# Kernel tuning notes

Hardware: AMD Instinct MI355X
Metric: run time of the kernel (lower is better)

Reference implementation:

```python
import jax, jax.numpy as jnp
import numpy as np

Y = 1      # init kwarg y
DIM = 2    # init kwarg dim


def setup_inputs() -> dict:
    key = jax.random.key(0)
    k1, k2, k3 = jax.random.split(key, 3)
    B, L = 16, 512
    H = 32
    x = jax.random.normal(k1, (B, L, L), dtype=jnp.float32)
    # xavier_uniform-like init for weights
    lim1 = np.sqrt(6.0 / (3 + H)).astype(np.float32)
    W1 = jax.random.uniform(k2, (H, 3), dtype=jnp.float32, minval=-lim1, maxval=lim1)
    b1 = jnp.zeros((H,), dtype=jnp.float32)
    lim2 = np.sqrt(6.0 / (H + 1)).astype(np.float32)
    W2 = jax.random.uniform(k3, (1, H), dtype=jnp.float32, minval=-lim2, maxval=lim2)
    b2 = jnp.zeros((1,), dtype=jnp.float32)
    return {"x": x, "W1": W1, "b1": b1, "W2": W2, "b2": b2}


def reference(x, W1, b1, W2, b2):
    # nearest-neighbor sum along both lattice dims
    x1 = (jnp.roll(x, 1, axis=1) + jnp.roll(x, -1, axis=1)
          + jnp.roll(x, 1, axis=2) + jnp.roll(x, -1, axis=2))
    # shifted-by-y neighbor sum along DIM
    sx = jnp.roll(x, Y, axis=DIM) + jnp.roll(x, -Y, axis=DIM)
    # per-site 3-feature vector: [x^2, x1*x, sx*x] -> (B, L, L, 3)
    inp = jnp.stack([x * x, x1 * x, sx * x], axis=-1)
    # tiny pointwise MLP 3 -> 32 -> 1
    h = jnp.tanh(jnp.einsum('blmf,hf->blmh', inp, W1) + b1)
    out = jnp.einsum('blmh,oh->blmo', h, W2)[..., 0] + b2[0]
    # sum over lattice sites -> per-config scalar (B,)
    return out.sum(axis=(1, 2))
```

## Files before the change

### kernel.cpp

```cpp
#include <hip/hip_runtime.h>

#define L 512
#define LMASK 511
#define HID 32

constexpr int THREADS        = 256;
constexpr int ROWS_PER_BLOCK = 4;
constexpr int BLOCKS_PER_B   = L / ROWS_PER_BLOCK;
constexpr int NTAB           = 680;
constexpr float UCLAMP_HI    = 672.99f;

__global__ __launch_bounds__(THREADS, 4)
void site_kernel(const float* __restrict__ x,
                 const float* __restrict__ W1,
                 const float* __restrict__ b1,
                 const float* __restrict__ W2,
                 float* __restrict__ partial) {
    __shared__ __align__(16) float  zw_s[128];
    __shared__ __align__(16) float  w2_s[HID];
    __shared__ __align__(8)  float2 tab_s[NTAB];

    const int t = threadIdx.x;

    if (t < HID) {
        const float K16 = 16.0f * 2.8853900817779268f;
        const int g = t >> 2, q = t & 3;
        zw_s[g * 16 +  0 + q] = K16 * W1[t * 3 + 0];
        zw_s[g * 16 +  4 + q] = K16 * W1[t * 3 + 1];
        zw_s[g * 16 +  8 + q] = K16 * W1[t * 3 + 2];
        zw_s[g * 16 + 12 + q] = fmaf(K16, b1[t], 336.0f);
        w2_s[t] = -2.0f * W2[t];
    }
    for (int i = t; i < NTAB; i += THREADS) {
        const float z0 = fmaf((float)i, 0.0625f, -21.0f);
        const float v0 = 1.0f / (1.0f + __builtin_amdgcn_exp2f(z0));
        const float v1 = 1.0f / (1.0f + __builtin_amdgcn_exp2f(z0 + 0.0625f));
        const float s  = v1 - v0;
        tab_s[i] = make_float2(s, fmaf(-s, (float)i, v0));
    }
    __syncthreads();

    const int blk = blockIdx.x;
    const int b   = blk >> 7;
    const int i0  = (blk & (BLOCKS_PER_B - 1)) * ROWS_PER_BLOCK;
    const float* __restrict__ xb = x + (size_t)b * (L * L);

    float F0[8], F1[8], F2[8];
#pragma unroll
    for (int g = 0; g < 2; ++g) {
        const int j  = t + g * THREADS;
        const int jm = (j + LMASK) & LMASK, jp = (j + 1) & LMASK;

        float cc[6];
#pragma unroll
        for (int r = 0; r < 6; ++r) {
            const int i = (i0 + r - 1 + L) & LMASK;
            cc[r] = xb[i * L + j];
        }
#pragma unroll
        for (int s = 0; s < 4; ++s) {
            const int i   = i0 + s;
            const float lf = xb[i * L + jm];
            const float rg = xb[i * L + jp];
            const float c  = cc[s + 1];
            const float lr = lf + rg;
            const float x1 = lr + cc[s] + cc[s + 2];
            const int k = g * 4 + s;
            F0[k] = c * c;  F1[k] = x1 * c;  F2[k] = lr * c;
        }
    }

    float acc[8] = {0.f, 0.f, 0.f, 0.f, 0.f, 0.f, 0.f, 0.f};

#pragma unroll 1
    for (int gq = 0; gq < 8; ++gq) {
        const float4 wa  = *(const float4*)&zw_s[gq * 16 + 0];
        const float4 wb  = *(const float4*)&zw_s[gq * 16 + 4];
        const float4 wc  = *(const float4*)&zw_s[gq * 16 + 8];
        const float4 w0  = *(const float4*)&zw_s[gq * 16 + 12];
        const float4 w2v = *(const float4*)&w2_s[gq * 4];
#pragma unroll
        for (int q = 0; q < 4; ++q) {
            const float waq = ((const float*)&wa)[q];
            const float wbq = ((const float*)&wb)[q];
            const float wcq = ((const float*)&wc)[q];
            const float w0q = ((const float*)&w0)[q];
            const float w2q = ((const float*)&w2v)[q];
#pragma unroll
            for (int s = 0; s < 8; ++s) {
                const float uu = fmaf(F0[s], waq, fmaf(F1[s], wbq, fmaf(F2[s], wcq, w0q)));
                const float uc = __builtin_amdgcn_fmed3f(uu, 0.0f, UCLAMP_HI);
                const int  idx = (int)uc;
                const float2 sa = tab_s[idx];
                acc[s] = fmaf(w2q, fmaf(sa.x, uc, sa.y), acc[s]);
            }
        }
    }

    float a = ((acc[0] + acc[1]) + (acc[2] + acc[3]))
            + ((acc[4] + acc[5]) + (acc[6] + acc[7]));
#pragma unroll
    for (int off = 32; off > 0; off >>= 1)
        a += __shfl_down(a, off, 64);

    __shared__ float wsum[THREADS / 64];
    const int wid = t >> 6, lane = t & 63;
    if (lane == 0) wsum[wid] = a;
    __syncthreads();
    if (t == 0)
        partial[blk] = (wsum[0] + wsum[1]) + (wsum[2] + wsum[3]);
}

__global__ __launch_bounds__(128)
void reduce_kernel(const float* __restrict__ partial,
                   const float* __restrict__ W2,
                   const float* __restrict__ b2,
                   float* __restrict__ out) {
    const int b = blockIdx.x, t = threadIdx.x;
    const float NS = (float)(L * L);

    float v = partial[b * BLOCKS_PER_B + t];
    if (t < HID) v += NS * W2[t];
    if (t == 0)  v += NS * b2[0];

#pragma unroll
    for (int off = 32; off > 0; off >>= 1)
        v += __shfl_down(v, off, 64);

    __shared__ float ws2[2];
    if ((t & 63) == 0) ws2[t >> 6] = v;
    __syncthreads();
    if (t == 0) out[b] = ws2[0] + ws2[1];
}

extern "C" void kernel_launch(void* const* d_in, const int* in_sizes, int n_in,
                              void* d_out, int out_size, void* d_ws, size_t ws_size,
                              hipStream_t stream) {
    const float* x  = (const float*)d_in[0];
    const float* W1 = (const float*)d_in[1];
    const float* b1 = (const float*)d_in[2];
    const float* W2 = (const float*)d_in[3];
    const float* b2 = (const float*)d_in[4];
    float* out      = (float*)d_out;
    float* partial  = (float*)d_ws;

    const int B = in_sizes[0] / (L * L);

    site_kernel<<<B * BLOCKS_PER_B, THREADS, 0, stream>>>(x, W1, b1, W2, partial);
    reduce_kernel<<<B, 128, 0, stream>>>(partial, W2, b2, out);
}
```

Measured before the change: 35.42 us.

## Replace interpolated tanh table with denser nearest-entry table via magic-number indexing

Swaps the 680-entry linear-interpolation sigmoid table for a 5376-entry nearest-neighbour table at 1/64 spacing. A magic-number bias (2^23) is added to the pre-activation so the table byte offset can be pulled straight from the float mantissa bits. This removes the float-to-int conversion, the float2 load and the interpolation FMA from the inner loop. In exchange, accuracy drops from linear interpolation to nearest-sample lookup, and shared memory use grows to about 21KB per block. The occupancy hint in launch_bounds is also removed.

```diff
diff --git a/kernel.cpp b/kernel.cpp
--- a/kernel.cpp
+++ b/kernel.cpp
@@ -7,36 +7,36 @@
 constexpr int THREADS        = 256;
 constexpr int ROWS_PER_BLOCK = 4;
 constexpr int BLOCKS_PER_B   = L / ROWS_PER_BLOCK;
-constexpr int NTAB           = 680;
-constexpr float UCLAMP_HI    = 672.99f;
+constexpr int NTAB           = 5376;
 
-__global__ __launch_bounds__(THREADS, 4)
+constexpr float MAGIC   = 8388608.0f;
+constexpr float CLAMPLO = 8388608.0f;
+constexpr float CLAMPHI = 8410108.0f;
+
+__global__ __launch_bounds__(THREADS)
 void site_kernel(const float* __restrict__ x,
                  const float* __restrict__ W1,
                  const float* __restrict__ b1,
                  const float* __restrict__ W2,
                  float* __restrict__ partial) {
-    __shared__ __align__(16) float  zw_s[128];
-    __shared__ __align__(16) float  w2_s[HID];
-    __shared__ __align__(8)  float2 tab_s[NTAB];
+    __shared__ __align__(16) float tab_s[NTAB];
+    __shared__ __align__(16) float zw_s[128];
+    __shared__ __align__(16) float w2_s[HID];
 
     const int t = threadIdx.x;
 
     if (t < HID) {
-        const float K16 = 16.0f * 2.8853900817779268f;
+        const float K256 = 256.0f * 2.8853900817779268f;
         const int g = t >> 2, q = t & 3;
-        zw_s[g * 16 +  0 + q] = K16 * W1[t * 3 + 0];
-        zw_s[g * 16 +  4 + q] = K16 * W1[t * 3 + 1];
-        zw_s[g * 16 +  8 + q] = K16 * W1[t * 3 + 2];
-        zw_s[g * 16 + 12 + q] = fmaf(K16, b1[t], 336.0f);
+        zw_s[g * 16 +  0 + q] = K256 * W1[t * 3 + 0];
+        zw_s[g * 16 +  4 + q] = K256 * W1[t * 3 + 1];
+        zw_s[g * 16 +  8 + q] = K256 * W1[t * 3 + 2];
+        zw_s[g * 16 + 12 + q] = fmaf(K256, b1[t], 5378.0f + MAGIC);
         w2_s[t] = -2.0f * W2[t];
     }
     for (int i = t; i < NTAB; i += THREADS) {
-        const float z0 = fmaf((float)i, 0.0625f, -21.0f);
-        const float v0 = 1.0f / (1.0f + __builtin_amdgcn_exp2f(z0));
-        const float v1 = 1.0f / (1.0f + __builtin_amdgcn_exp2f(z0 + 0.0625f));
-        const float s  = v1 - v0;
-        tab_s[i] = make_float2(s, fmaf(-s, (float)i, v0));
+        const float zp = fmaf((float)i, 0.015625f, -21.0f);
+        tab_s[i] = __builtin_amdgcn_rcpf(1.0f + __builtin_amdgcn_exp2f(zp));
     }
     __syncthreads();
 
@@ -71,6 +71,7 @@
     }
 
     float acc[8] = {0.f, 0.f, 0.f, 0.f, 0.f, 0.f, 0.f, 0.f};
+    const char* __restrict__ tb = (const char*)tab_s;
 
 #pragma unroll 1
     for (int gq = 0; gq < 8; ++gq) {
@@ -89,10 +90,10 @@
 #pragma unroll
             for (int s = 0; s < 8; ++s) {
                 const float uu = fmaf(F0[s], waq, fmaf(F1[s], wbq, fmaf(F2[s], wcq, w0q)));
-                const float uc = __builtin_amdgcn_fmed3f(uu, 0.0f, UCLAMP_HI);
-                const int  idx = (int)uc;
-                const float2 sa = tab_s[idx];
-                acc[s] = fmaf(w2q, fmaf(sa.x, uc, sa.y), acc[s]);
+                const float uc = __builtin_amdgcn_fmed3f(uu, CLAMPLO, CLAMPHI);
+                const int  off = __float_as_int(uc) & 0x007FFFFC;
+                const float y  = *reinterpret_cast<const float*>(tb + off);
+                acc[s] = fmaf(w2q, y, acc[s]);
             }
         }
     }
```

After: 35.58 us. About the same (+0.5%).
